# Performance work log

Measured on AMD Instinct MI355X. Metric: run time of the kernel, lower is better.

The kernel has to match this reference:

```python
import jax, jax.numpy as jnp
import numpy as np

HEADS = 8
EPS_LN = 1e-5
EPS_N = 1e-12


def _dw(x, w, b, pad):
    # depthwise conv, NCHW, weight [C,1,kh,kw]
    C = x.shape[1]
    y = jax.lax.conv_general_dilated(x, w, (1, 1), pad,
                                     dimension_numbers=('NCHW', 'OIHW', 'NCHW'),
                                     feature_group_count=C)
    return y + b[None, :, None, None]


def _pw(x, w, b):
    # 1x1 conv as einsum, weight [Cout, Cin]
    return jnp.einsum('bihw,oi->bohw', x, w) + b[None, :, None, None]


def _l2n(x):
    n = jnp.sqrt(jnp.sum(x * x, axis=-1, keepdims=True))
    return x / jnp.maximum(n, EPS_N)


def _axis_attn(q, k, v):
    # q,k,v: [B, heads, N, D]; L2-normalized QK, softmax, +q residual
    q = _l2n(q)
    k = _l2n(k)
    attn = jax.nn.softmax(jnp.einsum('bhnd,bhmd->bhnm', q, k), axis=-1)
    return jnp.einsum('bhnm,bhmd->bhnd', attn, v) + q


def setup_inputs() -> dict:
    key = jax.random.key(0)
    B, C, H, W = 16, 256, 80, 80
    ks = jax.random.split(key, 16)

    def nrm(k, shape, s=0.02):
        return jax.random.normal(k, shape, dtype=jnp.float32) * s

    z = lambda *s: jnp.zeros(s, jnp.float32)
    return {
        'x': nrm(ks[0], (B, C, H, W), 1.0),
        'ln_g': jnp.ones((C,), jnp.float32),
        'ln_b': z(C),
        'w_in': nrm(ks[1], (C, C)), 'b_in': z(C),
        'w_out': nrm(ks[2], (C, C)), 'b_out': z(C),
        'wx7': nrm(ks[3], (C, 1, 1, 7)), 'bx7': z(C),
        'wx11': nrm(ks[4], (C, 1, 1, 11)), 'bx11': z(C),
        'wx21': nrm(ks[5], (C, 1, 1, 21)), 'bx21': z(C),
        'wy7': nrm(ks[6], (C, 1, 7, 1)), 'by7': z(C),
        'wy11': nrm(ks[7], (C, 1, 11, 1)), 'by11': z(C),
        'wy21': nrm(ks[8], (C, 1, 21, 1)), 'by21': z(C),
    }


def reference(x, ln_g, ln_b, w_in, b_in, w_out, b_out,
              wx7, bx7, wx11, bx11, wx21, bx21,
              wy7, by7, wy11, by11, wy21, by21):
    B, C, H, W = x.shape
    cp = C // HEADS

    # LayerNorm over channel dim (applied per-pixel)
    mu = jnp.mean(x, axis=1, keepdims=True)
    var = jnp.var(x, axis=1, keepdims=True)
    xn = (x - mu) / jnp.sqrt(var + EPS_LN)
    xn = xn * ln_g[None, :, None, None] + ln_b[None, :, None, None]

    fx = _pw(_dw(xn, wx7, bx7, ((0, 0), (3, 3)))
             + _dw(xn, wx11, bx11, ((0, 0), (5, 5)))
             + _dw(xn, wx21, bx21, ((0, 0), (10, 10))), w_in, b_in)
    fy = _pw(_dw(xn, wy7, by7, ((3, 3), (0, 0)))
             + _dw(xn, wy11, by11, ((5, 5), (0, 0)))
             + _dw(xn, wy21, by21, ((10, 10), (0, 0))), w_in, b_in)

    def to_h(t):  # [B,C,H,W] -> [B,heads,H,W*cp] (w outer, c inner)
        return t.reshape(B, HEADS, cp, H, W).transpose(0, 1, 3, 4, 2).reshape(B, HEADS, H, W * cp)

    def from_h(t):
        return t.reshape(B, HEADS, H, W, cp).transpose(0, 1, 4, 2, 3).reshape(B, C, H, W)

    def to_w(t):  # [B,C,H,W] -> [B,heads,W,H*cp] (h outer, c inner)
        return t.reshape(B, HEADS, cp, H, W).transpose(0, 1, 4, 3, 2).reshape(B, HEADS, W, H * cp)

    def from_w(t):
        return t.reshape(B, HEADS, W, H, cp).transpose(0, 1, 4, 3, 2).reshape(B, C, H, W)

    out_x = from_h(_axis_attn(to_h(fy), to_h(fx), to_h(fx)))
    out_y = from_w(_axis_attn(to_w(fx), to_w(fy), to_w(fy)))

    return _pw(out_x, w_out, b_out) + _pw(out_y, w_out, b_out) + x
```

## Files before the change

### kernel.cpp

```cpp
#include <hip/hip_runtime.h>

typedef unsigned short u16;
typedef unsigned int   u32;

#define NB  16
#define NC  256
#define NH  80
#define NW  80
#define NHW 6400

typedef short bf16x8 __attribute__((ext_vector_type(8)));
typedef float f32x4  __attribute__((ext_vector_type(4)));

__device__ __forceinline__ float b2f(u16 u) {
  union { u32 i; float f; } c; c.i = ((u32)u) << 16; return c.f;
}
__device__ __forceinline__ u16 f2b(float f) {
  union { float f; u32 i; } c; c.f = f;
  return (u16)((c.i + 0x7FFFu + ((c.i >> 16) & 1u)) >> 16);
}
__device__ __forceinline__ float ldx(const void* p, size_t i, int f32f) {
  return f32f ? ((const float*)p)[i] : b2f(((const u16*)p)[i]);
}
__device__ __forceinline__ int getf(int fh, const int* flagp) {
  return (fh >= 0) ? fh : *flagp;
}

__global__ void probe_init(int* __restrict__ flag) { flag[0] = 0; flag[1] = 0; }

__global__ __launch_bounds__(256) void probe_count(const u16* __restrict__ x,
                                                   int* __restrict__ flag)
{
  __shared__ int cnt[256];
  int base = (blockIdx.x * 256 + threadIdx.x) * 16;
  int c = 0;
  uint4 v0 = *(const uint4*)(x + base);
  uint4 v1 = *(const uint4*)(x + base + 8);
  u32 w[8] = {v0.x, v0.y, v0.z, v0.w, v1.x, v1.y, v1.z, v1.w};
  #pragma unroll
  for (int j = 0; j < 8; j++) {
    if (((w[j] >> 7)  & 0xFFu) == 0xFFu) c++;
    if (((w[j] >> 23) & 0xFFu) == 0xFFu) c++;
  }
  cnt[threadIdx.x] = c; __syncthreads();
  for (int s = 128; s > 0; s >>= 1) {
    if (threadIdx.x < s) cnt[threadIdx.x] += cnt[threadIdx.x + s];
    __syncthreads();
  }
  if (threadIdx.x == 0) atomicAdd(&flag[1], cnt[0]);
}

__global__ void probe_decide(int* __restrict__ flag) {
  flag[0] = (flag[1] > 16) ? 1 : 0;
}

struct CvtArgs { const void* src[18]; int cum[19]; };

__global__ __launch_bounds__(256) void cvt_weights(CvtArgs a, float* __restrict__ dst,
                                                   int fh, const int* __restrict__ flagp)
{
  int f = getf(fh, flagp);
  int i = blockIdx.x * 256 + threadIdx.x;
  int s = 0;
  while (i >= a.cum[s + 1]) s++;
  int j = i - a.cum[s];
  float v = f ? ((const float*)a.src[s])[j] : b2f(((const u16*)a.src[s])[j]);
  if (!(v == v) || fabsf(v) > 1e30f) v = 0.f;
  dst[i] = v;
}

__global__ __launch_bounds__(256) void split_w(const float* __restrict__ w_in,
    const float* __restrict__ w_out, u16* __restrict__ WB)
{
  int i = blockIdx.x * 256 + threadIdx.x;
  int mat = i >> 16, idx = i & 65535;
  float v = (mat ? w_out : w_in)[idx];
  u16 hi = f2b(v);
  u16 lo = f2b(v - b2f(hi));
  WB[mat * 131072 + idx] = hi;
  WB[mat * 131072 + 65536 + idx] = lo;
}

__global__ __launch_bounds__(256) void ln_stats(const void* __restrict__ xsrc,
    size_t xoff, int fh, const int* __restrict__ flagp, float2* __restrict__ stats)
{
  int f = getf(fh, flagp);
  int bl = blockIdx.y;
  int p4 = blockIdx.x * 1024 + threadIdx.x * 4;
  if (p4 >= NHW) return;
  size_t base = xoff + (size_t)bl * NC * NHW + p4;
  float s1[4] = {0.f, 0.f, 0.f, 0.f}, s2[4] = {0.f, 0.f, 0.f, 0.f};
  if (f) {
    const float* xp = (const float*)xsrc + base;
    for (int c = 0; c < NC; c++) {
      float4 v = *(const float4*)(xp + (size_t)c * NHW);
      s1[0] += v.x; s2[0] += v.x * v.x;
      s1[1] += v.y; s2[1] += v.y * v.y;
      s1[2] += v.z; s2[2] += v.z * v.z;
      s1[3] += v.w; s2[3] += v.w * v.w;
    }
  } else {
    const u16* xp = (const u16*)xsrc + base;
    for (int c = 0; c < NC; c++) {
      ushort4 v = *(const ushort4*)(xp + (size_t)c * NHW);
      float a = b2f(v.x), b = b2f(v.y), cc = b2f(v.z), d = b2f(v.w);
      s1[0] += a;  s2[0] += a * a;
      s1[1] += b;  s2[1] += b * b;
      s1[2] += cc; s2[2] += cc * cc;
      s1[3] += d;  s2[3] += d * d;
    }
  }
  float2* so = stats + (size_t)bl * NHW + p4;
  #pragma unroll
  for (int j = 0; j < 4; j++) {
    float mean = s1[j] * (1.f / 256.f);
    float var  = s2[j] * (1.f / 256.f) - mean * mean;
    so[j] = make_float2(mean, rsqrtf(var + 1e-5f));
  }
}

__global__ __launch_bounds__(256) void dw_both(const void* __restrict__ xsrc,
    size_t xoff, int fh, const int* __restrict__ flagp,
    const float2* __restrict__ stats,
    const float* __restrict__ g, const float* __restrict__ bt,
    const float* __restrict__ wx7,  const float* __restrict__ bx7,
    const float* __restrict__ wx11, const float* __restrict__ bx11,
    const float* __restrict__ wx21, const float* __restrict__ bx21,
    const float* __restrict__ wy7,  const float* __restrict__ by7,
    const float* __restrict__ wy11, const float* __restrict__ by11,
    const float* __restrict__ wy21, const float* __restrict__ by21,
    u16* __restrict__ sx, u16* __restrict__ sy)
{
  __shared__ float xnp[80][116];
  __shared__ float cwx[21], cwy[21];
  __shared__ float cbs[2];
  int f = getf(fh, flagp);
  int bc = blockIdx.x;
  int c  = bc & 255;
  int bl = bc >> 8;
  int t = threadIdx.x;
  if (t < 21) {
    float v = wx21[c * 21 + t];
    if (t >= 5 && t <= 15) v += wx11[c * 11 + t - 5];
    if (t >= 7 && t <= 13) v += wx7[c * 7 + t - 7];
    cwx[t] = v;
  } else if (t < 42) {
    int j = t - 21;
    float v = wy21[c * 21 + j];
    if (j >= 5 && j <= 15) v += wy11[c * 11 + j - 5];
    if (j >= 7 && j <= 13) v += wy7[c * 7 + j - 7];
    cwy[j] = v;
  } else if (t == 42) { cbs[0] = bx7[c] + bx11[c] + bx21[c]; }
  else if (t == 43)   { cbs[1] = by7[c] + by11[c] + by21[c]; }
  for (int i = t; i < 2560; i += 256) {
    int rr = i >> 5, cc = i & 31;
    xnp[rr][cc < 16 ? cc : 80 + cc] = 0.f;
  }
  float cg = g[c], cbt = bt[c];
  size_t xrow = xoff + (size_t)bc * NHW;
  const float2* st = stats + (size_t)bl * NHW;
  for (int i = t; i < NHW; i += 256) {
    float v = ldx(xsrc, xrow + i, f);
    float2 s = st[i];
    xnp[i / 80][16 + i % 80] = (v - s.x) * s.y * cg + cbt;
  }
  __syncthreads();
  float bxv = cbs[0], byv = cbs[1];
  size_t obase = (size_t)bc * NHW;
  for (int u = t; u < 800; u += 256) {
    int h = u / 10, w0 = (u % 10) * 8;
    float r[32];
    #pragma unroll
    for (int j = 0; j < 8; j++)
      *(float4*)&r[4 * j] = *(const float4*)&xnp[h][w0 + 4 + 4 * j];
    float ax[8], ay[8];
    #pragma unroll
    for (int j = 0; j < 8; j++) { ax[j] = bxv; ay[j] = byv; }
    #pragma unroll
    for (int dd = 0; dd < 21; dd++) {
      float wv = cwx[dd];
      #pragma unroll
      for (int j = 0; j < 8; j++) ax[j] += wv * r[j + 2 + dd];
    }
    #pragma unroll
    for (int dd = 0; dd < 21; dd++) {
      int hp = h + dd - 10;
      int hc = min(max(hp, 0), 79);
      float wv = (hp == hc) ? cwy[dd] : 0.f;
      float4 v0 = *(const float4*)&xnp[hc][16 + w0];
      float4 v1 = *(const float4*)&xnp[hc][20 + w0];
      ay[0] += wv * v0.x; ay[1] += wv * v0.y; ay[2] += wv * v0.z; ay[3] += wv * v0.w;
      ay[4] += wv * v1.x; ay[5] += wv * v1.y; ay[6] += wv * v1.z; ay[7] += wv * v1.w;
    }
    size_t ob = obase + h * 80 + w0;
    ushort4 a0, a1, b0, b1;
    a0.x = f2b(ax[0]); a0.y = f2b(ax[1]); a0.z = f2b(ax[2]); a0.w = f2b(ax[3]);
    a1.x = f2b(ax[4]); a1.y = f2b(ax[5]); a1.z = f2b(ax[6]); a1.w = f2b(ax[7]);
    b0.x = f2b(ay[0]); b0.y = f2b(ay[1]); b0.z = f2b(ay[2]); b0.w = f2b(ay[3]);
    b1.x = f2b(ay[4]); b1.y = f2b(ay[5]); b1.z = f2b(ay[6]); b1.w = f2b(ay[7]);
    *(ushort4*)(sx + ob)     = a0;
    *(ushort4*)(sx + ob + 4) = a1;
    *(ushort4*)(sy + ob)     = b0;
    *(ushort4*)(sy + ob + 4) = b1;
  }
}

template<int FINAL>
__global__ __launch_bounds__(256) void pw_mfma_t(const u16* __restrict__ WB,
    u16* io0, u16* io1, const float* __restrict__ bias,
    void* __restrict__ OutBase, size_t out_off,
    const void* __restrict__ xsrc, size_t xoff,
    int fh, const int* __restrict__ flagp, int Nb, int chunk)
{
  __shared__ u16 S[16384];
  constexpr int MT = FINAL ? 2 : 4;
  int d = blockIdx.x;
  int w = chunk ? (d & 7) * chunk + (d >> 3) : d;
  int oh, px, bl, zz;
  if (FINAL) {
    oh = w & 1; int s = w >> 1; px = s % 50; bl = s / 50; zz = 0;
  } else {
    oh = 0; px = w % 50; int q = w / 50; bl = q % Nb; zz = q / Nb;
  }
  int p0 = px * 128;
  int t  = threadIdx.x;
  int lane = t & 63, wid = t >> 6, lg = lane >> 4, lr = lane & 15;
  u16* io = (FINAL || zz == 0) ? io0 : io1;

  f32x4 acc[MT][8];
  #pragma unroll
  for (int m = 0; m < MT; m++)
    #pragma unroll
    for (int n = 0; n < 8; n++)
      acc[m][n] = (f32x4){0.f, 0.f, 0.f, 0.f};

  for (int kh = 0; kh < 2; kh++) {
    if (kh) __syncthreads();
    {
      int kb = t >> 4, pb = t & 15;
      const u16* src = io + ((size_t)bl * NC + kh * 128 + kb * 8) * NHW + p0 + pb * 8;
      u32 r[8][4];
      #pragma unroll
      for (int i = 0; i < 8; i++) {
        uint4 v = *(const uint4*)(src + (size_t)i * NHW);
        r[i][0] = v.x; r[i][1] = v.y; r[i][2] = v.z; r[i][3] = v.w;
      }
      #pragma unroll
      for (int j = 0; j < 8; j++) {
        u32 wv[4];
        #pragma unroll
        for (int m = 0; m < 4; m++) {
          u32 a = r[2 * m][j >> 1], b = r[2 * m + 1][j >> 1];
          wv[m] = (j & 1) ? ((a >> 16) | (b & 0xFFFF0000u))
                          : ((a & 0xFFFFu) | (b << 16));
        }
        int pp = pb * 8 + j;
        int gg = ((pp >> 3) ^ pp) & 15;
        *(uint4*)&S[pp * 128 + ((kb ^ gg) & 15) * 8] = make_uint4(wv[0], wv[1], wv[2], wv[3]);
      }
    }
    __syncthreads();
    #pragma unroll
    for (int chl = 0; chl < 4; chl++) {
      int kglob = kh * 128 + chl * 32;
      #pragma unroll
      for (int m = 0; m < MT; m++) {
        int o = (FINAL ? oh * 128 : 0) + (wid * MT + m) * 16 + lr;
        const u16* wrow = WB + (size_t)o * 256 + kglob + lg * 8;
        bf16x8 ahi = *(const bf16x8*)(wrow);
        bf16x8 alo = *(const bf16x8*)(wrow + 65536);
        #pragma unroll
        for (int ng = 0; ng < 4; ng++) {
          int pxa = (ng * 2) * 16 + lr, pxb = pxa + 16;
          int ka = chl * 4 + lg;
          bf16x8 b0 = *(const bf16x8*)&S[pxa * 128 + ((ka ^ (((pxa >> 3) ^ pxa) & 15)) & 15) * 8];
          bf16x8 b1 = *(const bf16x8*)&S[pxb * 128 + ((ka ^ (((pxb >> 3) ^ pxb) & 15)) & 15) * 8];
          acc[m][ng * 2]     = __builtin_amdgcn_mfma_f32_16x16x32_bf16(ahi, b0, acc[m][ng * 2], 0, 0, 0);
          acc[m][ng * 2]     = __builtin_amdgcn_mfma_f32_16x16x32_bf16(alo, b0, acc[m][ng * 2], 0, 0, 0);
          acc[m][ng * 2 + 1] = __builtin_amdgcn_mfma_f32_16x16x32_bf16(ahi, b1, acc[m][ng * 2 + 1], 0, 0, 0);
          acc[m][ng * 2 + 1] = __builtin_amdgcn_mfma_f32_16x16x32_bf16(alo, b1, acc[m][ng * 2 + 1], 0, 0, 0);
        }
      }
    }
  }
  __syncthreads();

  if (FINAL) {
    float* Otf = (float*)S;
    int f = getf(fh, flagp);
    #pragma unroll
    for (int h = 0; h < 2; h++) {
      if ((wid >> 1) == h) {
        #pragma unroll
        for (int m = 0; m < 2; m++)
          #pragma unroll
          for (int r = 0; r < 4; r++) {
            int ol = (wid * 2 + m) * 16 + 4 * lg + r;
            int ro = ol & 63;
            float bv = 2.f * bias[oh * 128 + ol];
            #pragma unroll
            for (int n = 0; n < 8; n++) {
              int pxn = n * 16 + lr;
              int cuf = (pxn >> 2) ^ (ro & 7);
              Otf[ro * 128 + cuf * 4 + (pxn & 3)] = acc[m][n][r] + bv;
            }
          }
      }
      __syncthreads();
      int row = t >> 2, q = t & 3;
      size_t gbase = ((size_t)bl * NC + oh * 128 + h * 64 + row) * NHW + p0 + q * 32;
      #pragma unroll
      for (int j = 0; j < 8; j++) {
        int uf = q * 8 + j;
        int cuf = uf ^ (row & 7);
        float4 v = *(float4*)&Otf[row * 128 + cuf * 4];
        size_t gi = gbase + j * 4;
        if (f) {
          const float* xp = (const float*)xsrc + xoff + gi;
          v.x += xp[0]; v.y += xp[1]; v.z += xp[2]; v.w += xp[3];
          *(float4*)((float*)OutBase + out_off + gi) = v;
        } else {
          ushort4 xv = *(const ushort4*)((const u16*)xsrc + xoff + gi);
          ushort4 ov;
          ov.x = f2b(v.x + b2f(xv.x)); ov.y = f2b(v.y + b2f(xv.y));
          ov.z = f2b(v.z + b2f(xv.z)); ov.w = f2b(v.w + b2f(xv.w));
          *(ushort4*)((u16*)OutBase + out_off + gi) = ov;
        }
      }
      __syncthreads();
    }
  } else {
    u16* Ot = S;
    #pragma unroll
    for (int h = 0; h < 2; h++) {
      if ((wid >> 1) == h) {
        #pragma unroll
        for (int m = 0; m < 4; m++)
          #pragma unroll
          for (int r = 0; r < 4; r++) {
            int o  = (wid * 4 + m) * 16 + 4 * lg + r;
            int ol = o & 127;
            float bv = bias[o];
            #pragma unroll
            for (int n = 0; n < 8; n++) {
              int pxn = n * 16 + lr;
              int cu = ((pxn >> 3) + (ol & 7)) & 15;
              Ot[ol * 128 + cu * 8 + (pxn & 7)] = f2b(acc[m][n][r] + bv);
            }
          }
      }
      __syncthreads();
      int row = t >> 1, half = t & 1;
      u16* orow = io + ((size_t)bl * NC + h * 128 + row) * NHW + p0 + half * 64;
      #pragma unroll
      for (int j = 0; j < 8; j++) {
        int cu = ((half * 8 + j) + (row & 7)) & 15;
        *(uint4*)(orow + j * 8) = *(uint4*)&Ot[row * 128 + cu * 8];
      }
      __syncthreads();
    }
  }
  (void)OutBase; (void)out_off; (void)xsrc; (void)xoff; (void)flagp; (void)io1;
}

__global__ __launch_bounds__(256) void transpose_sumsq(const u16* __restrict__ fx,
    const u16* __restrict__ fy, u16* __restrict__ fxT, u16* __restrict__ fyT,
    float* __restrict__ rs_fx, float* __restrict__ rs_fy,
    float* __restrict__ cs_fx, float* __restrict__ cs_fy)
{
  __shared__ u16 tile[80][81];
  int pl = blockIdx.x, ten = blockIdx.y;
  const u16* src = (ten ? fy : fx) + (size_t)pl * NHW;
  u16*       dst = (ten ? fyT : fxT) + (size_t)pl * NHW;
  int t = threadIdx.x;
  for (int i = t; i < NHW; i += 256) tile[i / 80][i % 80] = src[i];
  __syncthreads();
  for (int i = t; i < NHW; i += 256) dst[i] = tile[i % 80][i / 80];
  if (t < 80) {
    float s = 0.f;
    #pragma unroll
    for (int k = 0; k < 80; k++) { float v = b2f(tile[t][k]); s += v * v; }
    (ten ? rs_fy : rs_fx)[pl * 80 + t] = s;
  } else if (t < 160) {
    int w = t - 80; float s = 0.f;
    #pragma unroll
    for (int h = 0; h < 80; h++) { float v = b2f(tile[h][w]); s += v * v; }
    (ten ? cs_fy : cs_fx)[pl * 80 + w] = s;
  }
}

__global__ __launch_bounds__(256) void norm_combine(const float* __restrict__ rs_fx,
    const float* __restrict__ rs_fy, const float* __restrict__ cs_fx,
    const float* __restrict__ cs_fy, float* __restrict__ invn, int Nb)
{
  int t = blockIdx.x * 256 + threadIdx.x;
  int blk = Nb * 640;
  int side = t / blk, r = t % blk;
  int b = r / 640, rem = r % 640, hd = rem / 80, row = rem % 80;
  const float* src = (side == 0) ? rs_fy : (side == 1) ? rs_fx : (side == 2) ? cs_fx : cs_fy;
  size_t base = (size_t)(b * 256 + hd * 32) * 80 + row;
  float s = 0.f;
  #pragma unroll
  for (int ci = 0; ci < 32; ci++) s += src[base + ci * 80];
  invn[t] = 1.f / fmaxf(sqrtf(s), 1e-12f);
}

template<int T0, int NT>
__device__ __forceinline__ void gram_wave(const u16* pa, const u16* pb,
                                          int lg, int lr, f32x4* acc)
{
  constexpr int MLO = T0 / 5;
  #pragma unroll
  for (int ch = 0; ch < 3; ch++) {
    bool tz = (ch == 2) && (lg >= 2);
    int kk = ch * 32 + 8 * lg;
    if (tz) kk = 0;
    bf16x8 af[2], bf[5];
    #pragma unroll
    for (int m = 0; m < 2; m++)
      af[m] = *(const bf16x8*)(pa + ((MLO + m) * 16 + lr) * 80 + kk);
    #pragma unroll
    for (int n = 0; n < 5; n++)
      bf[n] = *(const bf16x8*)(pb + (n * 16 + lr) * 80 + kk);
    if (tz) {
      bf16x8 z = {0, 0, 0, 0, 0, 0, 0, 0};
      af[0] = z; af[1] = z;
    }
    #pragma unroll
    for (int j = 0; j < NT; j++) {
      acc[j] = __builtin_amdgcn_mfma_f32_16x16x32_bf16(
          af[(T0 + j) / 5 - MLO], bf[(T0 + j) % 5], acc[j], 0, 0, 0);
    }
  }
}

template<int T0, int NT>
__device__ __forceinline__ void gram_all(const u16* Ab, const u16* Bb,
                                         int lg, int lr, f32x4* acc)
{
  for (int ci = 0; ci < 32; ci++)
    gram_wave<T0, NT>(Ab + (size_t)ci * NHW, Bb + (size_t)ci * NHW, lg, lr, acc);
}

__global__ __launch_bounds__(256) void gram_softmax_mfma(const u16* __restrict__ fx,
    const u16* __restrict__ fy, const u16* __restrict__ fxT, const u16* __restrict__ fyT,
    const float* __restrict__ invn, u16* __restrict__ Sbuf, int Nb)
{
  __shared__ float At[80][81];
  int hd = blockIdx.x, b = blockIdx.y, axis = blockIdx.z;
  size_t sl0 = (size_t)(b * 256 + hd * 32) * NHW;
  const u16* Ab = (axis ? fxT : fy) + sl0;
  const u16* Bb = (axis ? fyT : fx) + sl0;
  int t = threadIdx.x, lane = t & 63, wid = t >> 6;
  int lg = lane >> 4, lr = lane & 15;
  f32x4 acc0 = {0.f, 0.f, 0.f, 0.f};
  f32x4 acc[7];
  #pragma unroll
  for (int j = 0; j < 7; j++) acc[j] = acc0;
  if      (wid == 0) gram_all<0, 7>(Ab, Bb, lg, lr, acc);
  else if (wid == 1) gram_all<7, 6>(Ab, Bb, lg, lr, acc);
  else if (wid == 2) gram_all<13, 6>(Ab, Bb, lg, lr, acc);
  else               gram_all<19, 6>(Ab, Bb, lg, lr, acc);
  int blk = Nb * 640;
  int rowbase = (b * 8 + hd) * 80;
  const float* invq = invn + (axis ? 2 * blk : 0)   + rowbase;
  const float* invk = invn + (axis ? 3 * blk : blk) + rowbase;
  int t0  = wid ? 6 * wid + 1 : 0;
  int cnt = wid ? 6 : 7;
  #pragma unroll
  for (int j = 0; j < 7; j++) {
    if (j < cnt) {
      int tt = t0 + j, m = tt / 5, n = tt % 5;
      int col = n * 16 + lr;
      float ik = invk[col];
      #pragma unroll
      for (int r = 0; r < 4; r++) {
        int row = m * 16 + 4 * lg + r;
        float gv = acc[j][r] * invq[row] * ik;
        At[row][col] = fminf(fmaxf(gv, -8.f), 8.f);
      }
    }
  }
  __syncthreads();
  u16* Sg = Sbuf + ((size_t)(axis * Nb * 8 + b * 8 + hd)) * NHW;
  if (t < 80) {
    float mx = -1e30f;
    for (int j = 0; j < 80; j++) mx = fmaxf(mx, At[t][j]);
    float s = 0.f;
    for (int j = 0; j < 80; j++) s += __expf(At[t][j] - mx);
    float inv = 1.f / s;
    for (int j = 0; j < 80; j++) Sg[t * 80 + j] = f2b(__expf(At[t][j] - mx) * inv);
  }
}

template<int T0, int NT>
__device__ __forceinline__ void apply_wave(const u16* SH, const u16* fxT,
    const u16* fyP, const u16* SW, int lg, int lr, f32x4* acc)
{
  constexpr int MLO = T0 / 5;
  for (int ch = 0; ch < 3; ch++) {
    bool tz = (ch == 2) && (lg >= 2);
    int kk = ch * 32 + 8 * lg;
    if (tz) kk = 0;
    bf16x8 a1[2], a2[2], b1[5], b2[5];
    #pragma unroll
    for (int m = 0; m < 2; m++) {
      a1[m] = *(const bf16x8*)(SH  + ((MLO + m) * 16 + lr) * 80 + kk);
      a2[m] = *(const bf16x8*)(fyP + ((MLO + m) * 16 + lr) * 80 + kk);
    }
    #pragma unroll
    for (int n = 0; n < 5; n++) {
      b1[n] = *(const bf16x8*)(fxT + (n * 16 + lr) * 80 + kk);
      b2[n] = *(const bf16x8*)(SW  + (n * 16 + lr) * 80 + kk);
    }
    if (tz) {
      bf16x8 z = {0, 0, 0, 0, 0, 0, 0, 0};
      a1[0] = z; a1[1] = z; a2[0] = z; a2[1] = z;
    }
    #pragma unroll
    for (int j = 0; j < NT; j++) {
      acc[j] = __builtin_amdgcn_mfma_f32_16x16x32_bf16(
          a1[(T0 + j) / 5 - MLO], b1[(T0 + j) % 5], acc[j], 0, 0, 0);
      acc[j] = __builtin_amdgcn_mfma_f32_16x16x32_bf16(
          a2[(T0 + j) / 5 - MLO], b2[(T0 + j) % 5], acc[j], 0, 0, 0);
    }
  }
}

__global__ __launch_bounds__(256, 2) void apply_hw_mfma(const u16* __restrict__ fy_g,
    const u16* __restrict__ fxT_g, const u16* __restrict__ Sbuf,
    const float* __restrict__ invn, u16* fx_io, int Nb)
{
  int ci = blockIdx.x, hd = blockIdx.y, b = blockIdx.z;
  size_t off = (size_t)(b * 256 + hd * 32 + ci) * NHW;
  const u16* SgH = Sbuf + (size_t)(b * 8 + hd) * NHW;
  const u16* SgW = Sbuf + ((size_t)(Nb * 8) + b * 8 + hd) * NHW;
  const u16* fyP = fy_g + off;
  const u16* fxT = fxT_g + off;
  int t = threadIdx.x, lane = t & 63, wid = t >> 6;
  int lg = lane >> 4, lr = lane & 15;
  f32x4 acc0 = {0.f, 0.f, 0.f, 0.f};
  f32x4 acc[7];
  #pragma unroll
  for (int j = 0; j < 7; j++) acc[j] = acc0;
  if      (wid == 0) apply_wave<0, 7>(SgH, fxT, fyP, SgW, lg, lr, acc);
  else if (wid == 1) apply_wave<7, 6>(SgH, fxT, fyP, SgW, lg, lr, acc);
  else if (wid == 2) apply_wave<13, 6>(SgH, fxT, fyP, SgW, lg, lr, acc);
  else               apply_wave<19, 6>(SgH, fxT, fyP, SgW, lg, lr, acc);
  const float* invqH = invn + (b * 8 + hd) * 80;
  const float* invqW = invn + 2 * Nb * 640 + (b * 8 + hd) * 80;
  int t0  = wid ? 6 * wid + 1 : 0;
  int cnt = wid ? 6 : 7;
  #pragma unroll
  for (int j = 0; j < 7; j++) {
    if (j < cnt) {
      int tt = t0 + j, m = tt / 5, n = tt % 5;
      int col = n * 16 + lr;
      float ivW = invqW[col];
      #pragma unroll
      for (int r = 0; r < 4; r++) {
        int row = m * 16 + 4 * lg + r;
        size_t ix = off + row * 80 + col;
        float v = acc[j][r] + b2f(fy_g[ix]) * invqH[row] + b2f(fx_io[ix]) * ivW;
        fx_io[ix] = f2b(v);
      }
    }
  }
}

extern "C" void kernel_launch(void* const* d_in, const int* in_sizes, int n_in,
                              void* d_out, int out_size, void* d_ws, size_t ws_size,
                              hipStream_t stream) {
  const int wsz[18] = {256, 256, 65536, 256, 65536, 256,
                       1792, 256, 2816, 256, 5376, 256,
                       1792, 256, 2816, 256, 5376, 256};
  CvtArgs ca;
  int cum = 0;
  for (int i = 0; i < 18; i++) { ca.src[i] = d_in[i + 1]; ca.cum[i] = cum; cum += wsz[i]; }
  ca.cum[18] = cum;

  int hostf = -1;
  if (in_sizes && n_in > 0) {
    if      (in_sizes[0] == 104857600) hostf = 1;
    else if (in_sizes[0] == 52428800)  hostf = 0;
  }
  if (hostf < 0) {
    if      (out_size == 104857600) hostf = 1;
    else if (out_size == 52428800)  hostf = 0;
  }

  int Nb = 1;
  for (int cand = 16; cand >= 1; cand >>= 1) {
    size_t need = (size_t)cand * 13701120 + 614416 + 524288;
    if (need <= ws_size) { Nb = cand; break; }
  }
  char* p = (char*)d_ws;
  int*    flag  = (int*)p;    p += 16;
  float*  wbuf  = (float*)p;  p += 614400;
  u16*    wsplit= (u16*)p;    p += 524288;
  u16*    fxbuf = (u16*)p;    p += (size_t)Nb * 3276800;
  u16*    fybuf = (u16*)p;    p += (size_t)Nb * 3276800;
  u16*    fxT   = (u16*)p;    p += (size_t)Nb * 3276800;
  u16*    fyT   = (u16*)p;    p += (size_t)Nb * 3276800;
  float2* stats = (float2*)p; p += (size_t)Nb * 51200;
  float*  rs_fx = (float*)p;  p += (size_t)Nb * 81920;
  float*  rs_fy = (float*)p;  p += (size_t)Nb * 81920;
  float*  cs_fx = (float*)p;  p += (size_t)Nb * 81920;
  float*  cs_fy = (float*)p;  p += (size_t)Nb * 81920;
  float*  invn  = (float*)p;  p += (size_t)Nb * 10240;
  u16*    Sbuf  = (u16*)p;

  float* ln_g = wbuf + ca.cum[0];  float* ln_b = wbuf + ca.cum[1];
  float* w_in = wbuf + ca.cum[2];  float* b_in = wbuf + ca.cum[3];
  float* w_out= wbuf + ca.cum[4]; float* b_out= wbuf + ca.cum[5];
  float* wx7  = wbuf + ca.cum[6];  float* bx7  = wbuf + ca.cum[7];
  float* wx11 = wbuf + ca.cum[8];  float* bx11 = wbuf + ca.cum[9];
  float* wx21 = wbuf + ca.cum[10]; float* bx21 = wbuf + ca.cum[11];
  float* wy7  = wbuf + ca.cum[12]; float* by7  = wbuf + ca.cum[13];
  float* wy11 = wbuf + ca.cum[14]; float* by11 = wbuf + ca.cum[15];
  float* wy21 = wbuf + ca.cum[16]; float* by21 = wbuf + ca.cum[17];

  if (hostf < 0) {
    probe_init<<<dim3(1), dim3(1), 0, stream>>>(flag);
    probe_count<<<dim3(64), dim3(256), 0, stream>>>((const u16*)d_in[0], flag);
    probe_decide<<<dim3(1), dim3(1), 0, stream>>>(flag);
  }
  cvt_weights<<<dim3(600), dim3(256), 0, stream>>>(ca, wbuf, hostf, flag);
  split_w<<<dim3(512), dim3(256), 0, stream>>>(w_in, w_out, wsplit);

  int Gpw = 100 * Nb;
  int chunk = (Gpw % 8 == 0) ? Gpw / 8 : 0;

  for (int b0 = 0; b0 < NB; b0 += Nb) {
    size_t xoff = (size_t)b0 * NC * NHW;

    ln_stats<<<dim3(7, Nb), dim3(256), 0, stream>>>(d_in[0], xoff, hostf, flag, stats);
    dw_both<<<dim3(Nb * 256), dim3(256), 0, stream>>>(d_in[0], xoff, hostf, flag, stats,
        ln_g, ln_b, wx7, bx7, wx11, bx11, wx21, bx21,
        wy7, by7, wy11, by11, wy21, by21, fxbuf, fybuf);
    pw_mfma_t<0><<<dim3(Gpw), dim3(256), 0, stream>>>(wsplit, fxbuf, fybuf,
        b_in, nullptr, 0, nullptr, 0, hostf, flag, Nb, chunk);
    transpose_sumsq<<<dim3(Nb * 256, 2), dim3(256), 0, stream>>>(fxbuf, fybuf, fxT, fyT,
        rs_fx, rs_fy, cs_fx, cs_fy);
    norm_combine<<<dim3(10 * Nb), dim3(256), 0, stream>>>(rs_fx, rs_fy, cs_fx, cs_fy, invn, Nb);
    gram_softmax_mfma<<<dim3(8, Nb, 2), dim3(256), 0, stream>>>(fxbuf, fybuf, fxT, fyT, invn, Sbuf, Nb);
    apply_hw_mfma<<<dim3(32, 8, Nb), dim3(256), 0, stream>>>(fybuf, fxT, Sbuf, invn, fxbuf, Nb);
    pw_mfma_t<1><<<dim3(Gpw), dim3(256), 0, stream>>>(wsplit + 131072, fxbuf, nullptr,
        b_out, d_out, xoff, d_in[0], xoff, hostf, flag, Nb, chunk);
  }
  (void)in_sizes; (void)n_in; (void)out_size;
}
```

Measured before the change: 864.4 us.

## Split input pointwise GEMM over output halves and write out-of-place

The first pointwise MFMA kernel used to compute all 256 output channels per block in place, which forced a two-phase writeback with extra barriers and a 4x8 accumulator tile. Each block now computes 128 output channels, so the grid doubles, registers per thread drop (launch bounds now request 4 blocks per CU), and results go to separate output buffers instead of overwriting the input. The transposed buffers are reused as the new destination, and the downstream kernels' buffer arguments are permuted to match. The cost is that every block reloads the full input tile, so input reads and staging work double.

```diff
diff --git a/kernel.cpp b/kernel.cpp
--- a/kernel.cpp
+++ b/kernel.cpp
@@ -206,30 +206,33 @@
 }
 
 template<int FINAL>
-__global__ __launch_bounds__(256) void pw_mfma_t(const u16* __restrict__ WB,
-    u16* io0, u16* io1, const float* __restrict__ bias,
+__global__ __launch_bounds__(256, 4) void pw_mfma_t(const u16* __restrict__ WB,
+    const u16* __restrict__ in0, const u16* __restrict__ in1,
+    u16* __restrict__ wout0, u16* __restrict__ wout1,
+    const float* __restrict__ bias,
     void* __restrict__ OutBase, size_t out_off,
     const void* __restrict__ xsrc, size_t xoff,
     int fh, const int* __restrict__ flagp, int Nb, int chunk)
 {
   __shared__ u16 S[16384];
-  constexpr int MT = FINAL ? 2 : 4;
   int d = blockIdx.x;
   int w = chunk ? (d & 7) * chunk + (d >> 3) : d;
-  int oh, px, bl, zz;
-  if (FINAL) {
-    oh = w & 1; int s = w >> 1; px = s % 50; bl = s / 50; zz = 0;
-  } else {
-    oh = 0; px = w % 50; int q = w / 50; bl = q % Nb; zz = q / Nb;
-  }
+  int oh = w & 1;
+  int s  = w >> 1;
+  int px = s % 50;
+  int q  = s / 50;
+  int bl, zz;
+  if (FINAL) { bl = q; zz = 0; }
+  else       { bl = q % Nb; zz = q / Nb; }
+  const u16* io = (FINAL || zz == 0) ? in0 : in1;
+  u16* wo = (zz == 0) ? wout0 : wout1;
   int p0 = px * 128;
   int t  = threadIdx.x;
   int lane = t & 63, wid = t >> 6, lg = lane >> 4, lr = lane & 15;
-  u16* io = (FINAL || zz == 0) ? io0 : io1;
-
-  f32x4 acc[MT][8];
-  #pragma unroll
-  for (int m = 0; m < MT; m++)
+
+  f32x4 acc[2][8];
+  #pragma unroll
+  for (int m = 0; m < 2; m++)
     #pragma unroll
     for (int n = 0; n < 8; n++)
       acc[m][n] = (f32x4){0.f, 0.f, 0.f, 0.f};
@@ -264,8 +267,8 @@
     for (int chl = 0; chl < 4; chl++) {
       int kglob = kh * 128 + chl * 32;
       #pragma unroll
-      for (int m = 0; m < MT; m++) {
-        int o = (FINAL ? oh * 128 : 0) + (wid * MT + m) * 16 + lr;
+      for (int m = 0; m < 2; m++) {
+        int o = oh * 128 + (wid * 2 + m) * 16 + lr;
         const u16* wrow = WB + (size_t)o * 256 + kglob + lg * 8;
         bf16x8 ahi = *(const bf16x8*)(wrow);
         bf16x8 alo = *(const bf16x8*)(wrow + 65536);
@@ -307,11 +310,11 @@
           }
       }
       __syncthreads();
-      int row = t >> 2, q = t & 3;
-      size_t gbase = ((size_t)bl * NC + oh * 128 + h * 64 + row) * NHW + p0 + q * 32;
+      int row = t >> 2, qq = t & 3;
+      size_t gbase = ((size_t)bl * NC + oh * 128 + h * 64 + row) * NHW + p0 + qq * 32;
       #pragma unroll
       for (int j = 0; j < 8; j++) {
-        int uf = q * 8 + j;
+        int uf = qq * 8 + j;
         int cuf = uf ^ (row & 7);
         float4 v = *(float4*)&Otf[row * 128 + cuf * 4];
         size_t gi = gbase + j * 4;
@@ -332,35 +335,29 @@
   } else {
     u16* Ot = S;
     #pragma unroll
-    for (int h = 0; h < 2; h++) {
-      if ((wid >> 1) == h) {
+    for (int m = 0; m < 2; m++)
+      #pragma unroll
+      for (int r = 0; r < 4; r++) {
+        int ol = (wid * 2 + m) * 16 + 4 * lg + r;
+        float bv = bias[oh * 128 + ol];
         #pragma unroll
-        for (int m = 0; m < 4; m++)
-          #pragma unroll
-          for (int r = 0; r < 4; r++) {
-            int o  = (wid * 4 + m) * 16 + 4 * lg + r;
-            int ol = o & 127;
-            float bv = bias[o];
-            #pragma unroll
-            for (int n = 0; n < 8; n++) {
-              int pxn = n * 16 + lr;
-              int cu = ((pxn >> 3) + (ol & 7)) & 15;
-              Ot[ol * 128 + cu * 8 + (pxn & 7)] = f2b(acc[m][n][r] + bv);
-            }
-          }
-      }
-      __syncthreads();
-      int row = t >> 1, half = t & 1;
-      u16* orow = io + ((size_t)bl * NC + h * 128 + row) * NHW + p0 + half * 64;
-      #pragma unroll
-      for (int j = 0; j < 8; j++) {
-        int cu = ((half * 8 + j) + (row & 7)) & 15;
-        *(uint4*)(orow + j * 8) = *(uint4*)&Ot[row * 128 + cu * 8];
-      }
-      __syncthreads();
-    }
-  }
-  (void)OutBase; (void)out_off; (void)xsrc; (void)xoff; (void)flagp; (void)io1;
+        for (int n = 0; n < 8; n++) {
+          int pxn = n * 16 + lr;
+          int cu = ((pxn >> 3) + (ol & 7)) & 15;
+          Ot[ol * 128 + cu * 8 + (pxn & 7)] = f2b(acc[m][n][r] + bv);
+        }
+      }
+    __syncthreads();
+    int row = t >> 1, half = t & 1;
+    u16* orow = wo + ((size_t)bl * NC + oh * 128 + row) * NHW + p0 + half * 64;
+    #pragma unroll
+    for (int j = 0; j < 8; j++) {
+      int cu = ((half * 8 + j) + (row & 7)) & 15;
+      *(uint4*)(orow + j * 8) = *(uint4*)&Ot[row * 128 + cu * 8];
+    }
+  }
+  (void)OutBase; (void)out_off; (void)xsrc; (void)xoff; (void)flagp;
+  (void)in1; (void)wout0; (void)wout1; (void)wo;
 }
 
 __global__ __launch_bounds__(256) void transpose_sumsq(const u16* __restrict__ fx,
@@ -600,8 +597,8 @@
   u16*    wsplit= (u16*)p;    p += 524288;
   u16*    fxbuf = (u16*)p;    p += (size_t)Nb * 3276800;
   u16*    fybuf = (u16*)p;    p += (size_t)Nb * 3276800;
-  u16*    fxT   = (u16*)p;    p += (size_t)Nb * 3276800;
-  u16*    fyT   = (u16*)p;    p += (size_t)Nb * 3276800;
+  u16*    gxbuf = (u16*)p;    p += (size_t)Nb * 3276800;
+  u16*    gybuf = (u16*)p;    p += (size_t)Nb * 3276800;
   float2* stats = (float2*)p; p += (size_t)Nb * 51200;
   float*  rs_fx = (float*)p;  p += (size_t)Nb * 81920;
   float*  rs_fy = (float*)p;  p += (size_t)Nb * 81920;
@@ -628,8 +625,10 @@
   cvt_weights<<<dim3(600), dim3(256), 0, stream>>>(ca, wbuf, hostf, flag);
   split_w<<<dim3(512), dim3(256), 0, stream>>>(w_in, w_out, wsplit);
 
-  int Gpw = 100 * Nb;
-  int chunk = (Gpw % 8 == 0) ? Gpw / 8 : 0;
+  int G0 = 200 * Nb;
+  int G1 = 100 * Nb;
+  int chunk0 = (G0 % 8 == 0) ? G0 / 8 : 0;
+  int chunk1 = (G1 % 8 == 0) ? G1 / 8 : 0;
 
   for (int b0 = 0; b0 < NB; b0 += Nb) {
     size_t xoff = (size_t)b0 * NC * NHW;
@@ -638,15 +637,17 @@
     dw_both<<<dim3(Nb * 256), dim3(256), 0, stream>>>(d_in[0], xoff, hostf, flag, stats,
         ln_g, ln_b, wx7, bx7, wx11, bx11, wx21, bx21,
         wy7, by7, wy11, by11, wy21, by21, fxbuf, fybuf);
-    pw_mfma_t<0><<<dim3(Gpw), dim3(256), 0, stream>>>(wsplit, fxbuf, fybuf,
-        b_in, nullptr, 0, nullptr, 0, hostf, flag, Nb, chunk);
-    transpose_sumsq<<<dim3(Nb * 256, 2), dim3(256), 0, stream>>>(fxbuf, fybuf, fxT, fyT,
-        rs_fx, rs_fy, cs_fx, cs_fy);
+    pw_mfma_t<0><<<dim3(G0), dim3(256), 0, stream>>>(wsplit, fxbuf, fybuf,
+        gxbuf, gybuf, b_in, nullptr, 0, nullptr, 0, hostf, flag, Nb, chunk0);
+    transpose_sumsq<<<dim3(Nb * 256, 2), dim3(256), 0, stream>>>(gxbuf, gybuf,
+        fxbuf, fybuf, rs_fx, rs_fy, cs_fx, cs_fy);
     norm_combine<<<dim3(10 * Nb), dim3(256), 0, stream>>>(rs_fx, rs_fy, cs_fx, cs_fy, invn, Nb);
-    gram_softmax_mfma<<<dim3(8, Nb, 2), dim3(256), 0, stream>>>(fxbuf, fybuf, fxT, fyT, invn, Sbuf, Nb);
-    apply_hw_mfma<<<dim3(32, 8, Nb), dim3(256), 0, stream>>>(fybuf, fxT, Sbuf, invn, fxbuf, Nb);
-    pw_mfma_t<1><<<dim3(Gpw), dim3(256), 0, stream>>>(wsplit + 131072, fxbuf, nullptr,
-        b_out, d_out, xoff, d_in[0], xoff, hostf, flag, Nb, chunk);
+    gram_softmax_mfma<<<dim3(8, Nb, 2), dim3(256), 0, stream>>>(gxbuf, gybuf,
+        fxbuf, fybuf, invn, Sbuf, Nb);
+    apply_hw_mfma<<<dim3(32, 8, Nb), dim3(256), 0, stream>>>(gybuf, fxbuf, Sbuf,
+        invn, gxbuf, Nb);
+    pw_mfma_t<1><<<dim3(G1), dim3(256), 0, stream>>>(wsplit + 131072, gxbuf, nullptr,
+        nullptr, nullptr, b_out, d_out, xoff, d_in[0], xoff, hostf, flag, Nb, chunk1);
   }
   (void)in_sizes; (void)n_in; (void)out_size;
 }
```

Measured after the change: 1.017 ms. 17.7% more time.
